# Kernel tuning notes

Measured on AMD Instinct MI355X. Metric: run time of the kernel, lower is better.

## Reference

```python
import jax, jax.numpy as jnp
import numpy as np

B, L, D_MODEL, D_MEM = 4, 8192, 512, 512
SSM_DIM = D_MODEL + D_MEM


def setup_inputs() -> dict:
    key = jax.random.key(0)
    ks = jax.random.split(key, 4)
    s = 0.02
    return {
        "x": jax.random.normal(ks[0], (B, L, D_MODEL), dtype=jnp.float32),
        "W_av": jax.random.normal(ks[1], (4 * D_MEM, D_MODEL), dtype=jnp.float32) * s,
        "b_av": jnp.zeros((4 * D_MEM,), dtype=jnp.float32),
        "W_go": jax.random.normal(ks[2], (D_MODEL, SSM_DIM), dtype=jnp.float32) * s,
        "b_go": jnp.zeros((D_MODEL,), dtype=jnp.float32),
        "W_out": jax.random.normal(ks[3], (2 * D_MODEL, D_MODEL), dtype=jnp.float32) * s,
        "b_out": jnp.zeros((2 * D_MODEL,), dtype=jnp.float32),
    }


def reference(x, W_av, b_av, W_go, b_go, W_out, b_out):
    d = D_MEM
    b = x.shape[0]
    # alpha_v = Linear(d_model -> 4*d_memory) on x[:, :-1]
    av = jnp.einsum("bld,kd->blk", x[:, :-1], W_av) + b_av
    # NRU memory update: alpha+*v+ - alpha-*v-  (all nonlins default to identity)
    ms_inp = av[..., :d] * av[..., d:2 * d] - av[..., 2 * d:3 * d] * av[..., 3 * d:4 * d]
    # associative cumsum scan along length, prefixed with zero initial memory
    ms = jnp.cumsum(ms_inp, axis=1)
    m_init = jnp.zeros((b, 1, d), dtype=x.dtype)
    ms = jnp.concatenate([m_init, ms], axis=1)  # [b, L, d_memory]
    ssm_inp = jnp.concatenate([x, ms], axis=2)  # [b, L, ssm_dim]
    # SSM sublayer (external registry module) stubbed as identity
    ssm_out = ssm_inp
    y = jnp.einsum("blk,dk->bld", ssm_out, W_go) + b_go  # gated_out
    y = jax.nn.gelu(y, approximate=False)  # activation='gelu' (torch exact erf)
    z = jnp.einsum("bld,kd->blk", y, W_out) + b_out  # [b, L, 2*d_model]
    y = z[..., :D_MODEL] * jax.nn.sigmoid(z[..., D_MODEL:])
    return y
```

## Files before the change

### kernel.cpp

```cpp
#include <hip/hip_runtime.h>
#include <hip/hip_bf16.h>
#include <math.h>

#define B_SZ 4
#define L_SZ 8192
#define DM 512
#define DMEM 512
#define M1 (B_SZ * (L_SZ - 1))
#define M2 (B_SZ * L_SZ)

typedef _Float16 h16;
typedef __attribute__((ext_vector_type(2))) _Float16 f16x2;
typedef __attribute__((ext_vector_type(8))) _Float16 f16x8;
typedef __attribute__((ext_vector_type(4))) float f32x4;

#define MFMA16(a, b, c) __builtin_amdgcn_mfma_f32_16x16x32_f16((a), (b), (c), 0, 0, 0)
#define WAVES_EU(mn, mx) __attribute__((amdgpu_waves_per_eu(mn, mx)))

__device__ __forceinline__ void gl16(const void* g, void* l) {
    __builtin_amdgcn_global_load_lds(
        (const __attribute__((address_space(1))) void*)g,
        (__attribute__((address_space(3))) void*)l, 16, 0, 0);
}

__device__ __forceinline__ f16x8 lds_frag(const h16* base, int row, int col, int key) {
    return *(const f16x8*)((const char*)base + row * 128 + ((col * 2) ^ (key << 4)));
}

__device__ __forceinline__ void xcd_remap(int& bx, int& by) {
    int gx = gridDim.x, gy = gridDim.y;
    int nwg = gx * gy;
    int lin = blockIdx.y * gx + blockIdx.x;
    int chunk = nwg >> 3;
    int l = (lin & 7) * chunk + (lin >> 3);
    by = l % gy;
    bx = l / gy;
}

__global__ __launch_bounds__(256) void conv_x(
    const float* __restrict__ src, h16* __restrict__ dst)
{
    int i = blockIdx.x * 256 + threadIdx.x;
    int m = i >> 6, bb = i & 63;
    const float4* s = (const float4*)(src + (size_t)m * 512 + bb * 8);
    float4 v0 = s[0], v1 = s[1];
    float vv[8] = {v0.x, v0.y, v0.z, v0.w, v1.x, v1.y, v1.z, v1.w};
    f16x8 o;
    #pragma unroll
    for (int j = 0; j < 8; ++j) o[j] = (h16)vv[j];
    int db = bb ^ (m & 7);
    *(f16x8*)(dst + (size_t)m * 512 + db * 8) = o;
}

__global__ __launch_bounds__(256) void conv_wgo(
    const float* __restrict__ src, h16* __restrict__ h)
{
    int i = blockIdx.x * 256 + threadIdx.x;
    int r = i >> 7, bb = i & 127;
    const float4* s = (const float4*)(src + (size_t)r * 1024 + bb * 8);
    float4 v0 = s[0], v1 = s[1];
    float vv[8] = {v0.x, v0.y, v0.z, v0.w, v1.x, v1.y, v1.z, v1.w};
    f16x8 hh;
    #pragma unroll
    for (int j = 0; j < 8; ++j) hh[j] = (h16)vv[j];
    int db = bb ^ (r & 7);
    *(f16x8*)(h + (size_t)r * 1024 + db * 8) = hh;
}

__global__ __launch_bounds__(256) void pack_wav(
    const float* __restrict__ src, h16* __restrict__ h)
{
    int i = blockIdx.x * 256 + threadIdx.x;
    int P = i >> 6, bb = i & 63;
    int by = P >> 7, lo = P & 127;
    int half = lo >> 6, g = (lo >> 4) & 3, nl = lo & 15;
    int orig = g * 512 + by * 32 + half * 16 + nl;
    const float4* s = (const float4*)(src + (size_t)orig * 512 + bb * 8);
    float4 v0 = s[0], v1 = s[1];
    float vv[8] = {v0.x, v0.y, v0.z, v0.w, v1.x, v1.y, v1.z, v1.w};
    f16x8 hh;
    #pragma unroll
    for (int j = 0; j < 8; ++j) hh[j] = (h16)vv[j];
    int db = bb ^ (P & 7);
    *(f16x8*)(h + (size_t)P * 512 + db * 8) = hh;
}

__global__ __launch_bounds__(256) void pack_wout(
    const float* __restrict__ src, h16* __restrict__ h)
{
    int i = blockIdx.x * 256 + threadIdx.x;
    int P = i >> 6, bb = i & 63;
    int by = P >> 7, lo = P & 127;
    int chunk = lo >> 5, g = (lo >> 4) & 1, nl = lo & 15;
    int orig = g * 512 + by * 64 + chunk * 16 + nl;
    const float4* s = (const float4*)(src + (size_t)orig * 512 + bb * 8);
    float4 v0 = s[0], v1 = s[1];
    float vv[8] = {v0.x, v0.y, v0.z, v0.w, v1.x, v1.y, v1.z, v1.w};
    f16x8 hh;
    #pragma unroll
    for (int j = 0; j < 8; ++j) hh[j] = (h16)vv[j];
    int db = bb ^ (P & 7);
    *(f16x8*)(h + (size_t)P * 512 + db * 8) = hh;
}

__global__ __launch_bounds__(256) WAVES_EU(3, 3) void gemm_av_mfma(
    const h16* __restrict__ xh, const h16* __restrict__ Wh,
    const float* __restrict__ bav, float* __restrict__ ms_inp)
{
    __shared__ __align__(16) h16 As[128 * 64];
    __shared__ __align__(16) h16 Bh[128 * 64];

    int bx, by; xcd_remap(bx, by);
    const int tid = threadIdx.x, lane = tid & 63, w = tid >> 6;
    const int wm = (w & 1) * 64, wn = (w >> 1) * 64;
    const int bm = bx * 128;
    const int ln = lane & 15, ko = (lane >> 4) * 8;
    const int kb = ln & 7;
    char* lA = (char*)As; char* lH = (char*)Bh;
    const int wb = w * 1024;

    const char *aP[4], *hP[4];
    {
        const int r8 = lane >> 3, c16 = (lane & 7) * 16;
        #pragma unroll
        for (int i = 0; i < 4; ++i) {
            int row = i * 32 + w * 8 + r8;
            int mg = bm + row; if (mg > M1 - 1) mg = M1 - 1;
            size_t xr = (size_t)mg + (unsigned)mg / (L_SZ - 1);
            aP[i] = (const char*)xh + xr * (DM * 2) + c16;
            size_t br = (size_t)(by * 128 + row) * (DM * 2) + c16;
            hP[i] = (const char*)Wh + br;
        }
    }
    int ka[4];
    #pragma unroll
    for (int fm = 0; fm < 4; ++fm) {
        int m = bm + wm + fm * 16 + ln;
        int mg = m > M1 - 1 ? M1 - 1 : m;
        ka[fm] = (int)((mg + (unsigned)mg / (L_SZ - 1)) & 7);
    }

    f32x4 acc[4][4];
    #pragma unroll
    for (int i = 0; i < 4; ++i)
        #pragma unroll
        for (int j = 0; j < 4; ++j) acc[i][j] = (f32x4){0.f, 0.f, 0.f, 0.f};

#define STAGE_AV(aoff, boff) do { \
    gl16(aP[0] + (aoff), lA + 0 * 4096 + wb); gl16(hP[0] + (boff), lH + 0 * 4096 + wb); \
    gl16(aP[1] + (aoff), lA + 1 * 4096 + wb); gl16(hP[1] + (boff), lH + 1 * 4096 + wb); \
    gl16(aP[2] + (aoff), lA + 2 * 4096 + wb); gl16(hP[2] + (boff), lH + 2 * 4096 + wb); \
    gl16(aP[3] + (aoff), lA + 3 * 4096 + wb); gl16(hP[3] + (boff), lH + 3 * 4096 + wb); \
} while (0)

    STAGE_AV(0, 0);
    for (int kt = 0; kt < 8; ++kt) {
        asm volatile("s_waitcnt vmcnt(0)" ::: "memory");
        __syncthreads();
        #pragma unroll
        for (int s = 0; s < 2; ++s) {
            const int c = s * 32 + ko;
            f16x8 a[4];
            #pragma unroll
            for (int fm = 0; fm < 4; ++fm)
                a[fm] = lds_frag(As, wm + fm * 16 + ln, c, ka[fm]);
            #pragma unroll
            for (int fn = 0; fn < 4; ++fn) {
                f16x8 vh = lds_frag(Bh, wn + fn * 16 + ln, c, kb);
                #pragma unroll
                for (int fm = 0; fm < 4; ++fm)
                    acc[fm][fn] = MFMA16(a[fm], vh, acc[fm][fn]);
            }
        }
        __syncthreads();
        if (kt < 7) { int off = (kt + 1) * 128; STAGE_AV(off, off); }
    }
#undef STAGE_AV

    const int lm = (lane >> 4) * 4;
    const int nn = by * 32 + (wn >> 6) * 16 + ln;
    const float b0 = bav[nn], b1 = bav[nn + 512], b2 = bav[nn + 1024], b3 = bav[nn + 1536];
    #pragma unroll
    for (int fm = 0; fm < 4; ++fm) {
        #pragma unroll
        for (int i = 0; i < 4; ++i) {
            int m = bm + wm + fm * 16 + lm + i;
            if (m < M1) {
                float a0 = acc[fm][0][i] + b0;
                float a1 = acc[fm][1][i] + b1;
                float a2 = acc[fm][2][i] + b2;
                float a3 = acc[fm][3][i] + b3;
                ms_inp[(size_t)m * DMEM + nn] = a0 * a1 - a2 * a3;
            }
        }
    }
}

__global__ __launch_bounds__(256) void scan_pass1(
    const float* __restrict__ ms_inp, float* __restrict__ csum)
{
    int c = blockIdx.x, b = blockIdx.y;
    int l0 = c * 128;
    int len = min(128, (L_SZ - 1) - l0);
    int t = threadIdx.x;
    const float2* p = (const float2*)(ms_inp + ((size_t)b * (L_SZ - 1) + l0) * DMEM) + t;
    float2 s = make_float2(0.f, 0.f);
    for (int i = 0; i < len; ++i) {
        float2 v = p[(size_t)i * 256];
        s.x += v.x; s.y += v.y;
    }
    ((float2*)(csum + ((size_t)b * 64 + c) * DMEM))[t] = s;
}

__global__ __launch_bounds__(256) void scan_pass2(float* __restrict__ csum)
{
    int sid = blockIdx.x * 4 + (threadIdx.x >> 6);
    int lane = threadIdx.x & 63;
    int b = sid >> 9, d = sid & 511;
    float* p = csum + (size_t)b * 64 * DMEM + d;
    float v = p[(size_t)lane * DMEM];
    #pragma unroll
    for (int off = 1; off < 64; off <<= 1) {
        float t = __shfl_up(v, off, 64);
        if (lane >= off) v += t;
    }
    float ex = __shfl_up(v, 1, 64);
    if (lane == 0) ex = 0.f;
    p[(size_t)lane * DMEM] = ex;
}

__global__ __launch_bounds__(256) void scan_pass3(
    const float* __restrict__ ms_inp, const float* __restrict__ csum,
    h16* __restrict__ msh)
{
    int c = blockIdx.x, b = blockIdx.y;
    int l0 = c * 128;
    int len = min(128, (L_SZ - 1) - l0);
    int t = threadIdx.x;
    float2 run = ((const float2*)(csum + ((size_t)b * 64 + c) * DMEM))[t];
    const float2* p = (const float2*)(ms_inp + ((size_t)b * (L_SZ - 1) + l0) * DMEM) + t;
    const int bb = t >> 2;
    const int sub = (t & 3) * 4;
    if (c == 0) {
        f16x2 z = {(h16)0.f, (h16)0.f};
        *(f16x2*)((char*)(msh + (size_t)b * L_SZ * DMEM) + bb * 16 + sub) = z;
    }
    for (int i = 0; i < len; ++i) {
        float2 v = p[(size_t)i * 256];
        run.x += v.x; run.y += v.y;
        int m = b * L_SZ + l0 + 1 + i;
        int db = bb ^ (m & 7);
        f16x2 o = {(h16)run.x, (h16)run.y};
        *(f16x2*)((char*)(msh + (size_t)m * DMEM) + db * 16 + sub) = o;
    }
}

__global__ __launch_bounds__(256) WAVES_EU(3, 3) void gemm_go_mfma(
    const h16* __restrict__ xh, const h16* __restrict__ msh,
    const h16* __restrict__ Wh,
    const float* __restrict__ bgo, h16* __restrict__ yh)
{
    __shared__ __align__(16) h16 As[128 * 64];
    __shared__ __align__(16) h16 Bh[128 * 64];

    int bx, by; xcd_remap(bx, by);
    const int tid = threadIdx.x, lane = tid & 63, w = tid >> 6;
    const int wm = (w & 1) * 64, wn = (w >> 1) * 64;
    const int bm = bx * 128, bn = by * 128;
    const int ln = lane & 15, ko = (lane >> 4) * 8;
    const int kk = ln & 7;
    char* lA = (char*)As; char* lH = (char*)Bh;
    const int wb = w * 1024;

    const char *xP[4], *mP[4], *hP[4];
    {
        const int r8 = lane >> 3, c16 = (lane & 7) * 16;
        #pragma unroll
        for (int i = 0; i < 4; ++i) {
            int row = i * 32 + w * 8 + r8;
            size_t ar = (size_t)(bm + row) * (DM * 2) + c16;
            xP[i] = (const char*)xh + ar;
            mP[i] = (const char*)msh + ar;
            size_t br = (size_t)(bn + row) * (2 * DM * 2) + c16;
            hP[i] = (const char*)Wh + br;
        }
    }

    f32x4 acc[4][4];
    #pragma unroll
    for (int i = 0; i < 4; ++i)
        #pragma unroll
        for (int j = 0; j < 4; ++j) acc[i][j] = (f32x4){0.f, 0.f, 0.f, 0.f};

#define STAGE_GO(AP, aoff, boff) do { \
    gl16(AP[0] + (aoff), lA + 0 * 4096 + wb); gl16(hP[0] + (boff), lH + 0 * 4096 + wb); \
    gl16(AP[1] + (aoff), lA + 1 * 4096 + wb); gl16(hP[1] + (boff), lH + 1 * 4096 + wb); \
    gl16(AP[2] + (aoff), lA + 2 * 4096 + wb); gl16(hP[2] + (boff), lH + 2 * 4096 + wb); \
    gl16(AP[3] + (aoff), lA + 3 * 4096 + wb); gl16(hP[3] + (boff), lH + 3 * 4096 + wb); \
} while (0)

    STAGE_GO(xP, 0, 0);
    for (int kt = 0; kt < 16; ++kt) {
        asm volatile("s_waitcnt vmcnt(0)" ::: "memory");
        __syncthreads();
        #pragma unroll
        for (int s = 0; s < 2; ++s) {
            const int c = s * 32 + ko;
            f16x8 a[4];
            #pragma unroll
            for (int fm = 0; fm < 4; ++fm)
                a[fm] = lds_frag(As, wm + fm * 16 + ln, c, kk);
            #pragma unroll
            for (int fn = 0; fn < 4; ++fn) {
                f16x8 vh = lds_frag(Bh, wn + fn * 16 + ln, c, kk);
                #pragma unroll
                for (int fm = 0; fm < 4; ++fm)
                    acc[fm][fn] = MFMA16(a[fm], vh, acc[fm][fn]);
            }
        }
        __syncthreads();
        int nx = kt + 1;
        if (nx < 8)       { STAGE_GO(xP, nx * 128, nx * 128); }
        else if (nx < 16) { STAGE_GO(mP, (nx - 8) * 128, nx * 128); }
    }
#undef STAGE_GO

    const int lm = (lane >> 4) * 4;
    #pragma unroll
    for (int fm = 0; fm < 4; ++fm) {
        #pragma unroll
        for (int fn = 0; fn < 4; ++fn) {
            int n = bn + wn + fn * 16 + ln;
            float bias = bgo[n];
            #pragma unroll
            for (int i = 0; i < 4; ++i) {
                int m = bm + wm + fm * 16 + lm + i;
                float t = acc[fm][fn][i] + bias;
                float g = 0.5f * t * (1.0f + erff(t * 0.70710678118654752f));
                int nsw = (((n >> 3) ^ (m & 7)) << 3) | (n & 7);
                yh[(size_t)m * DM + nsw] = (h16)g;
            }
        }
    }
}

__global__ __launch_bounds__(256) WAVES_EU(3, 3) void gemm_out_mfma(
    const h16* __restrict__ yh, const h16* __restrict__ Wh,
    const float* __restrict__ bout, float* __restrict__ out)
{
    __shared__ __align__(16) h16 As[128 * 64];
    __shared__ __align__(16) h16 Bh[128 * 64];

    int bx, by; xcd_remap(bx, by);
    const int tid = threadIdx.x, lane = tid & 63, w = tid >> 6;
    const int wm = (w & 1) * 64, wn = (w >> 1) * 64;
    const int bm = bx * 128;
    const int ln = lane & 15, ko = (lane >> 4) * 8;
    const int kk = ln & 7;
    char* lA = (char*)As; char* lH = (char*)Bh;
    const int wb = w * 1024;

    const char *aP[4], *hP[4];
    {
        const int r8 = lane >> 3, c16 = (lane & 7) * 16;
        #pragma unroll
        for (int i = 0; i < 4; ++i) {
            int row = i * 32 + w * 8 + r8;
            aP[i] = (const char*)yh + (size_t)(bm + row) * (DM * 2) + c16;
            size_t br = (size_t)(by * 128 + row) * (DM * 2) + c16;
            hP[i] = (const char*)Wh + br;
        }
    }

    f32x4 acc[4][4];
    #pragma unroll
    for (int i = 0; i < 4; ++i)
        #pragma unroll
        for (int j = 0; j < 4; ++j) acc[i][j] = (f32x4){0.f, 0.f, 0.f, 0.f};

#define STAGE_OUT(aoff, boff) do { \
    gl16(aP[0] + (aoff), lA + 0 * 4096 + wb); gl16(hP[0] + (boff), lH + 0 * 4096 + wb); \
    gl16(aP[1] + (aoff), lA + 1 * 4096 + wb); gl16(hP[1] + (boff), lH + 1 * 4096 + wb); \
    gl16(aP[2] + (aoff), lA + 2 * 4096 + wb); gl16(hP[2] + (boff), lH + 2 * 4096 + wb); \
    gl16(aP[3] + (aoff), lA + 3 * 4096 + wb); gl16(hP[3] + (boff), lH + 3 * 4096 + wb); \
} while (0)

    STAGE_OUT(0, 0);
    for (int kt = 0; kt < 8; ++kt) {
        asm volatile("s_waitcnt vmcnt(0)" ::: "memory");
        __syncthreads();
        #pragma unroll
        for (int s = 0; s < 2; ++s) {
            const int c = s * 32 + ko;
            f16x8 a[4];
            #pragma unroll
            for (int fm = 0; fm < 4; ++fm)
                a[fm] = lds_frag(As, wm + fm * 16 + ln, c, kk);
            #pragma unroll
            for (int fn = 0; fn < 4; ++fn) {
                f16x8 vh = lds_frag(Bh, wn + fn * 16 + ln, c, kk);
                #pragma unroll
                for (int fm = 0; fm < 4; ++fm)
                    acc[fm][fn] = MFMA16(a[fm], vh, acc[fm][fn]);
            }
        }
        __syncthreads();
        if (kt < 7) { int off = (kt + 1) * 128; STAGE_OUT(off, off); }
    }
#undef STAGE_OUT

    const int lm = (lane >> 4) * 4;
    #pragma unroll
    for (int fm = 0; fm < 4; ++fm) {
        #pragma unroll
        for (int cp = 0; cp < 2; ++cp) {
            int ncol = by * 64 + ((wn >> 5) + cp) * 16 + ln;
            float bz0 = bout[ncol], bz1 = bout[ncol + 512];
            #pragma unroll
            for (int i = 0; i < 4; ++i) {
                int m = bm + wm + fm * 16 + lm + i;
                float z0 = acc[fm][cp * 2 + 0][i] + bz0;
                float z1 = acc[fm][cp * 2 + 1][i] + bz1;
                out[(size_t)m * DM + ncol] = z0 * (1.0f / (1.0f + expf(-z1)));
            }
        }
    }
}

extern "C" void kernel_launch(void* const* d_in, const int* in_sizes, int n_in,
                              void* d_out, int out_size, void* d_ws, size_t ws_size,
                              hipStream_t stream)
{
    const float* x    = (const float*)d_in[0];
    const float* Wav  = (const float*)d_in[1];
    const float* bav  = (const float*)d_in[2];
    const float* Wgo  = (const float*)d_in[3];
    const float* bgo  = (const float*)d_in[4];
    const float* Wout = (const float*)d_in[5];
    const float* bout = (const float*)d_in[6];
    float* out = (float*)d_out;

    char* ws = (char*)d_ws;
    const size_t MB = 1 << 20;
    float* ms_inp = (float*)ws;
    h16*   yh     = (h16*)ws;
    h16*   xh     = (h16*)(ws + 64 * MB);
    h16*   msh    = (h16*)(ws + 96 * MB);
    float* csum   = (float*)(ws + 128 * MB);
    h16*   Wavh   = (h16*)(ws + 129 * MB);
    h16*   Wgoh   = (h16*)(ws + 131 * MB);
    h16*   Wouth  = (h16*)(ws + 132 * MB);

    conv_x   <<<8192, 256, 0, stream>>>(x, xh);
    conv_wgo <<<256,  256, 0, stream>>>(Wgo, Wgoh);
    pack_wav <<<512,  256, 0, stream>>>(Wav, Wavh);
    pack_wout<<<256,  256, 0, stream>>>(Wout, Wouth);
    gemm_av_mfma<<<dim3(256, 16), 256, 0, stream>>>(xh, Wavh, bav, ms_inp);
    scan_pass1<<<dim3(64, B_SZ), 256, 0, stream>>>(ms_inp, csum);
    scan_pass2<<<512, 256, 0, stream>>>(csum);
    scan_pass3<<<dim3(64, B_SZ), 256, 0, stream>>>(ms_inp, csum, msh);
    gemm_go_mfma<<<dim3(256, 4), 256, 0, stream>>>(xh, msh, Wgoh, bgo, yh);
    gemm_out_mfma<<<dim3(256, 8), 256, 0, stream>>>(yh, Wouth, bout, out);
}
```

Baseline: 288.0 us.

## Double-buffer LDS in all three MFMA GEMMs and merge weight pack kernels

Each of the three GEMM kernels now keeps two LDS stages and prefetches tile kt+2 while computing tile kt. Partial vmcnt waits replace the full drain, so global-to-LDS loads overlap with MFMA work. This doubles LDS use per block, and the occupancy hint drops from 3 to 2 waves per EU, which risks losing latency hiding from fewer resident blocks. The three weight conversion kernels are also merged into one launch to cut launch overhead.

```diff
diff --git a/kernel.cpp b/kernel.cpp
--- a/kernel.cpp
+++ b/kernel.cpp
@@ -52,63 +52,60 @@
     *(f16x8*)(dst + (size_t)m * 512 + db * 8) = o;
 }
 
-__global__ __launch_bounds__(256) void conv_wgo(
-    const float* __restrict__ src, h16* __restrict__ h)
+__global__ __launch_bounds__(256) void pack_weights(
+    const float* __restrict__ Wgo, const float* __restrict__ Wav,
+    const float* __restrict__ Wout, h16* __restrict__ Wgoh,
+    h16* __restrict__ Wavh, h16* __restrict__ Wouth)
 {
     int i = blockIdx.x * 256 + threadIdx.x;
-    int r = i >> 7, bb = i & 127;
-    const float4* s = (const float4*)(src + (size_t)r * 1024 + bb * 8);
-    float4 v0 = s[0], v1 = s[1];
+    const float* s;
+    h16* d;
+    if (i < 65536) {
+        int r = i >> 7, bb = i & 127;
+        s = Wgo + (size_t)r * 1024 + bb * 8;
+        d = Wgoh + (size_t)r * 1024 + (bb ^ (r & 7)) * 8;
+    } else if (i < 196608) {
+        int j = i - 65536;
+        int P = j >> 6, bb = j & 63;
+        int by = P >> 7, lo = P & 127;
+        int half = lo >> 6, g = (lo >> 4) & 3, nl = lo & 15;
+        int orig = g * 512 + by * 32 + half * 16 + nl;
+        s = Wav + (size_t)orig * 512 + bb * 8;
+        d = Wavh + (size_t)P * 512 + (bb ^ (P & 7)) * 8;
+    } else {
+        int j = i - 196608;
+        int P = j >> 6, bb = j & 63;
+        int by = P >> 7, lo = P & 127;
+        int chunk = lo >> 5, g = (lo >> 4) & 1, nl = lo & 15;
+        int orig = g * 512 + by * 64 + chunk * 16 + nl;
+        s = Wout + (size_t)orig * 512 + bb * 8;
+        d = Wouth + (size_t)P * 512 + (bb ^ (P & 7)) * 8;
+    }
+    const float4* sv = (const float4*)s;
+    float4 v0 = sv[0], v1 = sv[1];
     float vv[8] = {v0.x, v0.y, v0.z, v0.w, v1.x, v1.y, v1.z, v1.w};
     f16x8 hh;
     #pragma unroll
     for (int j = 0; j < 8; ++j) hh[j] = (h16)vv[j];
-    int db = bb ^ (r & 7);
-    *(f16x8*)(h + (size_t)r * 1024 + db * 8) = hh;
-}
-
-__global__ __launch_bounds__(256) void pack_wav(
-    const float* __restrict__ src, h16* __restrict__ h)
-{
-    int i = blockIdx.x * 256 + threadIdx.x;
-    int P = i >> 6, bb = i & 63;
-    int by = P >> 7, lo = P & 127;
-    int half = lo >> 6, g = (lo >> 4) & 3, nl = lo & 15;
-    int orig = g * 512 + by * 32 + half * 16 + nl;
-    const float4* s = (const float4*)(src + (size_t)orig * 512 + bb * 8);
-    float4 v0 = s[0], v1 = s[1];
-    float vv[8] = {v0.x, v0.y, v0.z, v0.w, v1.x, v1.y, v1.z, v1.w};
-    f16x8 hh;
-    #pragma unroll
-    for (int j = 0; j < 8; ++j) hh[j] = (h16)vv[j];
-    int db = bb ^ (P & 7);
-    *(f16x8*)(h + (size_t)P * 512 + db * 8) = hh;
-}
-
-__global__ __launch_bounds__(256) void pack_wout(
-    const float* __restrict__ src, h16* __restrict__ h)
-{
-    int i = blockIdx.x * 256 + threadIdx.x;
-    int P = i >> 6, bb = i & 63;
-    int by = P >> 7, lo = P & 127;
-    int chunk = lo >> 5, g = (lo >> 4) & 1, nl = lo & 15;
-    int orig = g * 512 + by * 64 + chunk * 16 + nl;
-    const float4* s = (const float4*)(src + (size_t)orig * 512 + bb * 8);
-    float4 v0 = s[0], v1 = s[1];
-    float vv[8] = {v0.x, v0.y, v0.z, v0.w, v1.x, v1.y, v1.z, v1.w};
-    f16x8 hh;
-    #pragma unroll
-    for (int j = 0; j < 8; ++j) hh[j] = (h16)vv[j];
-    int db = bb ^ (P & 7);
-    *(f16x8*)(h + (size_t)P * 512 + db * 8) = hh;
-}
-
-__global__ __launch_bounds__(256) WAVES_EU(3, 3) void gemm_av_mfma(
+    *(f16x8*)d = hh;
+}
+
+#define PIPE_WAIT(N) do { \
+    asm volatile("s_waitcnt vmcnt(" #N ")" ::: "memory"); \
+    __builtin_amdgcn_s_barrier(); \
+    asm volatile("" ::: "memory"); \
+} while (0)
+#define PIPE_POST() do { \
+    __builtin_amdgcn_s_barrier(); \
+    asm volatile("" ::: "memory"); \
+} while (0)
+
+__global__ __launch_bounds__(256) WAVES_EU(2, 2) void gemm_av_mfma(
     const h16* __restrict__ xh, const h16* __restrict__ Wh,
     const float* __restrict__ bav, float* __restrict__ ms_inp)
 {
-    __shared__ __align__(16) h16 As[128 * 64];
-    __shared__ __align__(16) h16 Bh[128 * 64];
+    __shared__ __align__(16) h16 As[2][128 * 64];
+    __shared__ __align__(16) h16 Bh[2][128 * 64];
 
     int bx, by; xcd_remap(bx, by);
     const int tid = threadIdx.x, lane = tid & 63, w = tid >> 6;
@@ -116,7 +113,6 @@
     const int bm = bx * 128;
     const int ln = lane & 15, ko = (lane >> 4) * 8;
     const int kb = ln & 7;
-    char* lA = (char*)As; char* lH = (char*)Bh;
     const int wb = w * 1024;
 
     const char *aP[4], *hP[4];
@@ -146,34 +142,37 @@
         #pragma unroll
         for (int j = 0; j < 4; ++j) acc[i][j] = (f32x4){0.f, 0.f, 0.f, 0.f};
 
-#define STAGE_AV(aoff, boff) do { \
-    gl16(aP[0] + (aoff), lA + 0 * 4096 + wb); gl16(hP[0] + (boff), lH + 0 * 4096 + wb); \
-    gl16(aP[1] + (aoff), lA + 1 * 4096 + wb); gl16(hP[1] + (boff), lH + 1 * 4096 + wb); \
-    gl16(aP[2] + (aoff), lA + 2 * 4096 + wb); gl16(hP[2] + (boff), lH + 2 * 4096 + wb); \
-    gl16(aP[3] + (aoff), lA + 3 * 4096 + wb); gl16(hP[3] + (boff), lH + 3 * 4096 + wb); \
+#define STAGE_AV(koff, sel) do { \
+    char* dA = (char*)As[sel]; char* dB = (char*)Bh[sel]; \
+    gl16(aP[0] + (koff), dA + 0 * 4096 + wb); gl16(hP[0] + (koff), dB + 0 * 4096 + wb); \
+    gl16(aP[1] + (koff), dA + 1 * 4096 + wb); gl16(hP[1] + (koff), dB + 1 * 4096 + wb); \
+    gl16(aP[2] + (koff), dA + 2 * 4096 + wb); gl16(hP[2] + (koff), dB + 2 * 4096 + wb); \
+    gl16(aP[3] + (koff), dA + 3 * 4096 + wb); gl16(hP[3] + (koff), dB + 3 * 4096 + wb); \
 } while (0)
 
     STAGE_AV(0, 0);
+    STAGE_AV(128, 1);
     for (int kt = 0; kt < 8; ++kt) {
-        asm volatile("s_waitcnt vmcnt(0)" ::: "memory");
-        __syncthreads();
+        if (kt < 7) PIPE_WAIT(8); else PIPE_WAIT(0);
+        const h16* A = As[kt & 1];
+        const h16* B = Bh[kt & 1];
         #pragma unroll
         for (int s = 0; s < 2; ++s) {
             const int c = s * 32 + ko;
             f16x8 a[4];
             #pragma unroll
             for (int fm = 0; fm < 4; ++fm)
-                a[fm] = lds_frag(As, wm + fm * 16 + ln, c, ka[fm]);
+                a[fm] = lds_frag(A, wm + fm * 16 + ln, c, ka[fm]);
             #pragma unroll
             for (int fn = 0; fn < 4; ++fn) {
-                f16x8 vh = lds_frag(Bh, wn + fn * 16 + ln, c, kb);
+                f16x8 vh = lds_frag(B, wn + fn * 16 + ln, c, kb);
                 #pragma unroll
                 for (int fm = 0; fm < 4; ++fm)
                     acc[fm][fn] = MFMA16(a[fm], vh, acc[fm][fn]);
             }
         }
-        __syncthreads();
-        if (kt < 7) { int off = (kt + 1) * 128; STAGE_AV(off, off); }
+        PIPE_POST();
+        if (kt + 2 < 8) STAGE_AV((kt + 2) * 128, kt & 1);
     }
 #undef STAGE_AV
 
@@ -255,13 +254,13 @@
     }
 }
 
-__global__ __launch_bounds__(256) WAVES_EU(3, 3) void gemm_go_mfma(
+__global__ __launch_bounds__(256) WAVES_EU(2, 2) void gemm_go_mfma(
     const h16* __restrict__ xh, const h16* __restrict__ msh,
     const h16* __restrict__ Wh,
     const float* __restrict__ bgo, h16* __restrict__ yh)
 {
-    __shared__ __align__(16) h16 As[128 * 64];
-    __shared__ __align__(16) h16 Bh[128 * 64];
+    __shared__ __align__(16) h16 As[2][128 * 64];
+    __shared__ __align__(16) h16 Bh[2][128 * 64];
 
     int bx, by; xcd_remap(bx, by);
     const int tid = threadIdx.x, lane = tid & 63, w = tid >> 6;
@@ -269,7 +268,6 @@
     const int bm = bx * 128, bn = by * 128;
     const int ln = lane & 15, ko = (lane >> 4) * 8;
     const int kk = ln & 7;
-    char* lA = (char*)As; char* lH = (char*)Bh;
     const int wb = w * 1024;
 
     const char *xP[4], *mP[4], *hP[4];
@@ -292,36 +290,47 @@
         #pragma unroll
         for (int j = 0; j < 4; ++j) acc[i][j] = (f32x4){0.f, 0.f, 0.f, 0.f};
 
-#define STAGE_GO(AP, aoff, boff) do { \
-    gl16(AP[0] + (aoff), lA + 0 * 4096 + wb); gl16(hP[0] + (boff), lH + 0 * 4096 + wb); \
-    gl16(AP[1] + (aoff), lA + 1 * 4096 + wb); gl16(hP[1] + (boff), lH + 1 * 4096 + wb); \
-    gl16(AP[2] + (aoff), lA + 2 * 4096 + wb); gl16(hP[2] + (boff), lH + 2 * 4096 + wb); \
-    gl16(AP[3] + (aoff), lA + 3 * 4096 + wb); gl16(hP[3] + (boff), lH + 3 * 4096 + wb); \
+#define STAGE_GO(tt, sel) do { \
+    char* dA = (char*)As[sel]; char* dB = (char*)Bh[sel]; \
+    const int bo = (tt) * 128; \
+    if ((tt) < 8) { \
+        const int ao = (tt) * 128; \
+        gl16(xP[0] + ao, dA + 0 * 4096 + wb); gl16(hP[0] + bo, dB + 0 * 4096 + wb); \
+        gl16(xP[1] + ao, dA + 1 * 4096 + wb); gl16(hP[1] + bo, dB + 1 * 4096 + wb); \
+        gl16(xP[2] + ao, dA + 2 * 4096 + wb); gl16(hP[2] + bo, dB + 2 * 4096 + wb); \
+        gl16(xP[3] + ao, dA + 3 * 4096 + wb); gl16(hP[3] + bo, dB + 3 * 4096 + wb); \
+    } else { \
+        const int ao = ((tt) - 8) * 128; \
+        gl16(mP[0] + ao, dA + 0 * 4096 + wb); gl16(hP[0] + bo, dB + 0 * 4096 + wb); \
+        gl16(mP[1] + ao, dA + 1 * 4096 + wb); gl16(hP[1] + bo, dB + 1 * 4096 + wb); \
+        gl16(mP[2] + ao, dA + 2 * 4096 + wb); gl16(hP[2] + bo, dB + 2 * 4096 + wb); \
+        gl16(mP[3] + ao, dA + 3 * 4096 + wb); gl16(hP[3] + bo, dB + 3 * 4096 + wb); \
+    } \
 } while (0)
 
-    STAGE_GO(xP, 0, 0);
+    STAGE_GO(0, 0);
+    STAGE_GO(1, 1);
     for (int kt = 0; kt < 16; ++kt) {
-        asm volatile("s_waitcnt vmcnt(0)" ::: "memory");
-        __syncthreads();
+        if (kt < 15) PIPE_WAIT(8); else PIPE_WAIT(0);
+        const h16* A = As[kt & 1];
+        const h16* B = Bh[kt & 1];
         #pragma unroll
         for (int s = 0; s < 2; ++s) {
             const int c = s * 32 + ko;
             f16x8 a[4];
             #pragma unroll
             for (int fm = 0; fm < 4; ++fm)
-                a[fm] = lds_frag(As, wm + fm * 16 + ln, c, kk);
+                a[fm] = lds_frag(A, wm + fm * 16 + ln, c, kk);
             #pragma unroll
             for (int fn = 0; fn < 4; ++fn) {
-                f16x8 vh = lds_frag(Bh, wn + fn * 16 + ln, c, kk);
+                f16x8 vh = lds_frag(B, wn + fn * 16 + ln, c, kk);
                 #pragma unroll
                 for (int fm = 0; fm < 4; ++fm)
                     acc[fm][fn] = MFMA16(a[fm], vh, acc[fm][fn]);
             }
         }
-        __syncthreads();
-        int nx = kt + 1;
-        if (nx < 8)       { STAGE_GO(xP, nx * 128, nx * 128); }
-        else if (nx < 16) { STAGE_GO(mP, (nx - 8) * 128, nx * 128); }
+        PIPE_POST();
+        if (kt + 2 < 16) STAGE_GO(kt + 2, kt & 1);
     }
 #undef STAGE_GO
 
@@ -344,12 +353,12 @@
     }
 }
 
-__global__ __launch_bounds__(256) WAVES_EU(3, 3) void gemm_out_mfma(
+__global__ __launch_bounds__(256) WAVES_EU(2, 2) void gemm_out_mfma(
     const h16* __restrict__ yh, const h16* __restrict__ Wh,
     const float* __restrict__ bout, float* __restrict__ out)
 {
-    __shared__ __align__(16) h16 As[128 * 64];
-    __shared__ __align__(16) h16 Bh[128 * 64];
+    __shared__ __align__(16) h16 As[2][128 * 64];
+    __shared__ __align__(16) h16 Bh[2][128 * 64];
 
     int bx, by; xcd_remap(bx, by);
     const int tid = threadIdx.x, lane = tid & 63, w = tid >> 6;
@@ -357,7 +366,6 @@
     const int bm = bx * 128;
     const int ln = lane & 15, ko = (lane >> 4) * 8;
     const int kk = ln & 7;
-    char* lA = (char*)As; char* lH = (char*)Bh;
     const int wb = w * 1024;
 
     const char *aP[4], *hP[4];
@@ -378,34 +386,37 @@
         #pragma unroll
         for (int j = 0; j < 4; ++j) acc[i][j] = (f32x4){0.f, 0.f, 0.f, 0.f};
 
-#define STAGE_OUT(aoff, boff) do { \
-    gl16(aP[0] + (aoff), lA + 0 * 4096 + wb); gl16(hP[0] + (boff), lH + 0 * 4096 + wb); \
-    gl16(aP[1] + (aoff), lA + 1 * 4096 + wb); gl16(hP[1] + (boff), lH + 1 * 4096 + wb); \
-    gl16(aP[2] + (aoff), lA + 2 * 4096 + wb); gl16(hP[2] + (boff), lH + 2 * 4096 + wb); \
-    gl16(aP[3] + (aoff), lA + 3 * 4096 + wb); gl16(hP[3] + (boff), lH + 3 * 4096 + wb); \
+#define STAGE_OUT(koff, sel) do { \
+    char* dA = (char*)As[sel]; char* dB = (char*)Bh[sel]; \
+    gl16(aP[0] + (koff), dA + 0 * 4096 + wb); gl16(hP[0] + (koff), dB + 0 * 4096 + wb); \
+    gl16(aP[1] + (koff), dA + 1 * 4096 + wb); gl16(hP[1] + (koff), dB + 1 * 4096 + wb); \
+    gl16(aP[2] + (koff), dA + 2 * 4096 + wb); gl16(hP[2] + (koff), dB + 2 * 4096 + wb); \
+    gl16(aP[3] + (koff), dA + 3 * 4096 + wb); gl16(hP[3] + (koff), dB + 3 * 4096 + wb); \
 } while (0)
 
     STAGE_OUT(0, 0);
+    STAGE_OUT(128, 1);
     for (int kt = 0; kt < 8; ++kt) {
-        asm volatile("s_waitcnt vmcnt(0)" ::: "memory");
-        __syncthreads();
+        if (kt < 7) PIPE_WAIT(8); else PIPE_WAIT(0);
+        const h16* A = As[kt & 1];
+        const h16* B = Bh[kt & 1];
         #pragma unroll
         for (int s = 0; s < 2; ++s) {
             const int c = s * 32 + ko;
             f16x8 a[4];
             #pragma unroll
             for (int fm = 0; fm < 4; ++fm)
-                a[fm] = lds_frag(As, wm + fm * 16 + ln, c, kk);
+                a[fm] = lds_frag(A, wm + fm * 16 + ln, c, kk);
             #pragma unroll
             for (int fn = 0; fn < 4; ++fn) {
-                f16x8 vh = lds_frag(Bh, wn + fn * 16 + ln, c, kk);
+                f16x8 vh = lds_frag(B, wn + fn * 16 + ln, c, kk);
                 #pragma unroll
                 for (int fm = 0; fm < 4; ++fm)
                     acc[fm][fn] = MFMA16(a[fm], vh, acc[fm][fn]);
             }
         }
-        __syncthreads();
-        if (kt < 7) { int off = (kt + 1) * 128; STAGE_OUT(off, off); }
+        PIPE_POST();
+        if (kt + 2 < 8) STAGE_OUT((kt + 2) * 128, kt & 1);
     }
 #undef STAGE_OUT
 
@@ -451,10 +462,8 @@
     h16*   Wgoh   = (h16*)(ws + 131 * MB);
     h16*   Wouth  = (h16*)(ws + 132 * MB);
 
-    conv_x   <<<8192, 256, 0, stream>>>(x, xh);
-    conv_wgo <<<256,  256, 0, stream>>>(Wgo, Wgoh);
-    pack_wav <<<512,  256, 0, stream>>>(Wav, Wavh);
-    pack_wout<<<256,  256, 0, stream>>>(Wout, Wouth);
+    conv_x      <<<8192, 256, 0, stream>>>(x, xh);
+    pack_weights<<<1024, 256, 0, stream>>>(Wgo, Wav, Wout, Wgoh, Wavh, Wouth);
     gemm_av_mfma<<<dim3(256, 16), 256, 0, stream>>>(xh, Wavh, bav, ms_inp);
     scan_pass1<<<dim3(64, B_SZ), 256, 0, stream>>>(ms_inp, csum);
     scan_pass2<<<512, 256, 0, stream>>>(csum);
```

Result: faster. 277.2 us (-3.8%).
